# Optimization experiments

Hardware: AMD Instinct MI355X
Metric: run time of the kernel (lower is better)

Reference implementation:

```python
import jax, jax.numpy as jnp
import numpy as np

B = 2
D_MODEL = 768
N_HEADS = 16
N_POINTS = 4
SHAPES = [(16, 16), (32, 32), (64, 64), (96, 96)]  # (H, W) per level; query = last level
EPS = 1e-6


def layernorm(x, g, b):
    m = jnp.mean(x, -1, keepdims=True)
    xc = x - m
    v = jnp.mean(xc * xc, -1, keepdims=True)
    return xc * jax.lax.rsqrt(v + EPS) * g + b


def _bilinear(vflat, H, W, px, py):
    # vflat: (B, h, H*W, D); px/py: (B, Lq, h, P) unnormalized pixel coords
    # Equivalent to F.grid_sample(align_corners=False, padding_mode='zeros').
    x0f = jnp.floor(px); y0f = jnp.floor(py)
    lx = px - x0f; ly = py - y0f
    x0 = x0f.astype(jnp.int32); y0 = y0f.astype(jnp.int32)

    def gather(xi, yi, w):
        valid = ((xi >= 0) & (xi < W) & (yi >= 0) & (yi < H)).astype(vflat.dtype)
        idx = jnp.clip(yi, 0, H - 1) * W + jnp.clip(xi, 0, W - 1)
        idx = jnp.transpose(idx, (0, 2, 1, 3))        # (B, h, Lq, P)
        wv = jnp.transpose(w * valid, (0, 2, 1, 3))   # (B, h, Lq, P)
        b_, h_, q_, p_ = idx.shape
        g = jnp.take_along_axis(vflat, idx.reshape(b_, h_, q_ * p_)[..., None], axis=2)
        return g.reshape(b_, h_, q_, p_, -1) * wv[..., None]

    return (gather(x0, y0, (1 - lx) * (1 - ly)) + gather(x0 + 1, y0, lx * (1 - ly))
            + gather(x0, y0 + 1, (1 - lx) * ly) + gather(x0 + 1, y0 + 1, lx * ly))


def ms_deform_attn(query, ref_pts, feat, shapes, Wv, bv, Woff, boff, Wa, ba, Wo, bo):
    # query: (B, Lq, C); ref_pts: (1, Lq, 1, 2) in [0,1]; feat: (B, Lin, C)
    Bq, Lq, C = query.shape
    L, h, P = len(shapes), N_HEADS, N_POINTS
    D = C // h
    value = (feat @ Wv + bv).reshape(Bq, -1, h, D)
    off = (query @ Woff + boff).reshape(Bq, Lq, h, L, P, 2)
    w = jax.nn.softmax((query @ Wa + ba).reshape(Bq, Lq, h, L * P), axis=-1)
    w = w.reshape(Bq, Lq, h, L, P)
    normalizer = jnp.array([[W_, H_] for (H_, W_) in shapes], dtype=query.dtype)  # (L, 2) = [W, H]
    loc = ref_pts[:, :, None, :, None, :] + off / normalizer[None, None, None, :, None, :]
    out = jnp.zeros((Bq, h, Lq, D), query.dtype)
    start = 0
    for l, (H_, W_) in enumerate(shapes):
        vl = jnp.transpose(value[:, start:start + H_ * W_], (0, 2, 1, 3))  # (B, h, HW, D)
        start += H_ * W_
        px = loc[:, :, :, l, :, 0] * W_ - 0.5
        py = loc[:, :, :, l, :, 1] * H_ - 0.5
        samp = _bilinear(vl, H_, W_, px, py)                   # (B, h, Lq, P, D)
        wl = jnp.transpose(w[:, :, :, l, :], (0, 2, 1, 3))     # (B, h, Lq, P)
        out = out + jnp.einsum('bhqpd,bhqp->bhqd', samp, wl)
    out = jnp.transpose(out, (0, 2, 1, 3)).reshape(Bq, Lq, C)
    return out @ Wo + bo


def ref_points(e, dtype=jnp.float32):
    # torch.linspace(0.5, e-0.5, e)/e == (arange(e)+0.5)/e
    lin = (jnp.arange(e, dtype=dtype) + 0.5) / e
    ry, rx = jnp.meshgrid(lin, lin, indexing='ij')
    return jnp.stack([rx.ravel(), ry.ravel()], -1)[None, :, None, :]  # (1, e*e, 1, 2)


def setup_inputs() -> dict:
    key = jax.random.key(0)
    ks = jax.random.split(key, 16)
    d, h, P = D_MODEL, N_HEADS, N_POINTS
    inp = {}
    for i, (name, (H_, W_)) in enumerate(zip(['src0', 'src1', 'src2', 'src3'], SHAPES)):
        inp[name] = jax.random.normal(ks[i], (B, H_ * W_, d), jnp.float32)
    for pre in ('qn', 'fn', 'n1'):
        inp[pre + '_g'] = jnp.ones((d,), jnp.float32)
        inp[pre + '_b'] = jnp.zeros((d,), jnp.float32)
    inp['gamma1'] = 0.1 * jnp.ones((d,), jnp.float32)
    inp['gamma2'] = 0.1 * jnp.ones((d,), jnp.float32)

    def lin(k, din, dout):
        return jax.random.normal(k, (din, dout), jnp.float32) * (din ** -0.5)

    inp['c_Wv'] = lin(ks[4], d, d);               inp['c_bv'] = jnp.zeros((d,), jnp.float32)
    inp['c_Woff'] = lin(ks[5], d, h * 4 * P * 2); inp['c_boff'] = jnp.zeros((h * 4 * P * 2,), jnp.float32)
    inp['c_Wa'] = lin(ks[6], d, h * 4 * P);       inp['c_ba'] = jnp.zeros((h * 4 * P,), jnp.float32)
    inp['c_Wo'] = lin(ks[7], d, d);               inp['c_bo'] = jnp.zeros((d,), jnp.float32)
    inp['s_Wv'] = lin(ks[8], d, d);               inp['s_bv'] = jnp.zeros((d,), jnp.float32)
    inp['s_Woff'] = lin(ks[9], d, h * P * 2);     inp['s_boff'] = jnp.zeros((h * P * 2,), jnp.float32)
    inp['s_Wa'] = lin(ks[10], d, h * P);          inp['s_ba'] = jnp.zeros((h * P,), jnp.float32)
    inp['s_Wo'] = lin(ks[11], d, d);              inp['s_bo'] = jnp.zeros((d,), jnp.float32)
    return inp


def reference(src0, src1, src2, src3, qn_g, qn_b, fn_g, fn_b, n1_g, n1_b,
              gamma1, gamma2,
              c_Wv, c_bv, c_Woff, c_boff, c_Wa, c_ba, c_Wo, c_bo,
              s_Wv, s_bv, s_Woff, s_boff, s_Wa, s_ba, s_Wo, s_bo):
    feat = jnp.concatenate([src0, src1, src2, src3], axis=1)
    query = src3  # query_layer = -1
    e = SHAPES[-1][0]
    ref = ref_points(e, query.dtype)
    attn = ms_deform_attn(layernorm(query, qn_g, qn_b), ref, layernorm(feat, fn_g, fn_b),
                          SHAPES, c_Wv, c_bv, c_Woff, c_boff, c_Wa, c_ba, c_Wo, c_bo)
    attn1 = layernorm(attn, n1_g, n1_b)
    attn2 = ms_deform_attn(attn1, ref, attn1, [SHAPES[-1]],
                           s_Wv, s_bv, s_Woff, s_boff, s_Wa, s_ba, s_Wo, s_bo)
    attn = attn + gamma2 * attn2
    return query + gamma1 * attn
```

## Files before the change

kernel.cpp:

```cpp
#include <hip/hip_runtime.h>
#include <stdint.h>

typedef unsigned short u16;
typedef __attribute__((ext_vector_type(8))) __bf16 bf16x8;
typedef __attribute__((ext_vector_type(4))) float f32x4;
typedef __attribute__((ext_vector_type(2))) float f32x2;
typedef __attribute__((ext_vector_type(8))) u16 u16x8;
typedef __attribute__((ext_vector_type(4))) u16 u16x4;

#define DEV __device__ __forceinline__

DEV u16 f2b(float f) {
  union { float f; uint32_t u; } v; v.f = f;
  uint32_t u = v.u;
  return (u16)((u + 0x7fffu + ((u >> 16) & 1u)) >> 16);
}
DEV float b2f(u16 h) {
  union { uint32_t u; float f; } v; v.u = ((uint32_t)h) << 16;
  return v.f;
}
DEV float u2f(uint32_t u) {
  union { uint32_t u; float f; } v; v.u = u;
  return v.f;
}
DEV uint8_t f2fp8(float f) {
  return (uint8_t)(__builtin_amdgcn_cvt_pk_fp8_f32(f, f, 0, false) & 0xff);
}
DEV void fma16f8(f32x2* acc, uint4 v, float w) {
  f32x2 wv = {w, w};
  const uint32_t* pv = (const uint32_t*)&v;
  #pragma unroll
  for (int j = 0; j < 4; ++j) {
    f32x2 lo = __builtin_amdgcn_cvt_pk_f32_fp8(pv[j], false);
    f32x2 hi = __builtin_amdgcn_cvt_pk_f32_fp8(pv[j], true);
    acc[2 * j]     += wv * lo;
    acc[2 * j + 1] += wv * hi;
  }
}

__global__ __launch_bounds__(256) void wconv_kernel(
    const float* __restrict__ W0, const float* __restrict__ W1,
    const float* __restrict__ W2, const float* __restrict__ W3,
    const float* __restrict__ W4, const float* __restrict__ W5,
    const float* __restrict__ W6, const float* __restrict__ W7,
    u16* __restrict__ dst) {
  __shared__ float s[32][33];
  int bx = blockIdx.x;
  int ct = bx / 24;
  int kt = bx - ct * 24;
  const float* Wsrc; int N; int rowbase; int c0;
  if (ct < 24)       { Wsrc = W0; N = 768; rowbase = 0;    c0 = ct; }
  else if (ct < 40)  { Wsrc = W1; N = 512; rowbase = 768;  c0 = ct - 24; }
  else if (ct < 48)  { Wsrc = W2; N = 256; rowbase = 1280; c0 = ct - 40; }
  else if (ct < 72)  { Wsrc = W3; N = 768; rowbase = 1536; c0 = ct - 48; }
  else if (ct < 96)  { Wsrc = W4; N = 768; rowbase = 2304; c0 = ct - 72; }
  else if (ct < 100) { Wsrc = W5; N = 128; rowbase = 3072; c0 = ct - 96; }
  else if (ct < 104) { Wsrc = W6; N = 64;  rowbase = 3200; c0 = ct - 100; }
  else               { Wsrc = W7; N = 768; rowbase = 3328; c0 = ct - 104; }
  const int tx = threadIdx.x & 31, ty = threadIdx.x >> 5;
  const int n = c0 * 32 + tx;
  const int k0 = kt * 32;
  #pragma unroll
  for (int j = 0; j < 4; ++j) {
    int k = k0 + ty + j * 8;
    s[ty + j * 8][tx] = (n < N) ? Wsrc[(size_t)k * N + n] : 0.0f;
  }
  __syncthreads();
  #pragma unroll
  for (int j = 0; j < 4; ++j) {
    int nr = c0 * 32 + ty + j * 8;
    dst[(size_t)(rowbase + nr) * 768 + k0 + tx] = f2b(s[tx][ty + j * 8]);
  }
}

DEV void ln_core(float4 v, const float* __restrict__ g, const float* __restrict__ b,
                 u16* __restrict__ o, int t, float* red) {
  float s = v.x + v.y + v.z + v.w;
  float s2 = v.x * v.x + v.y * v.y + v.z * v.z + v.w * v.w;
  #pragma unroll
  for (int m = 1; m < 64; m <<= 1) { s += __shfl_xor(s, m); s2 += __shfl_xor(s2, m); }
  if ((t & 63) == 0) { red[t >> 6] = s; red[3 + (t >> 6)] = s2; }
  __syncthreads();
  float S = red[0] + red[1] + red[2];
  float S2 = red[3] + red[4] + red[5];
  float mean = S * (1.0f / 768.0f);
  float var = S2 * (1.0f / 768.0f) - mean * mean;
  float rstd = rsqrtf(var + 1e-6f);
  float4 gv = ((const float4*)g)[t], bv = ((const float4*)b)[t];
  u16x4 ov;
  ov[0] = f2b((v.x - mean) * rstd * gv.x + bv.x);
  ov[1] = f2b((v.y - mean) * rstd * gv.y + bv.y);
  ov[2] = f2b((v.z - mean) * rstd * gv.z + bv.z);
  ov[3] = f2b((v.w - mean) * rstd * gv.w + bv.w);
  *(u16x4*)(o + t * 4) = ov;
}

__global__ __launch_bounds__(192) void ln_rows_kernel(const float* __restrict__ in,
    const float* __restrict__ g, const float* __restrict__ b, u16* __restrict__ out) {
  __shared__ float red[6];
  size_t row = blockIdx.x;
  int t = threadIdx.x;
  ln_core(((const float4*)(in + row * 768))[t], g, b, out + row * 768, t, red);
}

__global__ __launch_bounds__(192) void ln_rows_b16_kernel(const u16* __restrict__ in,
    const float* __restrict__ g, const float* __restrict__ b, u16* __restrict__ out) {
  __shared__ float red[6];
  size_t row = blockIdx.x;
  int t = threadIdx.x;
  u16x4 r = *(const u16x4*)(in + row * 768 + t * 4);
  float4 v = {b2f(r[0]), b2f(r[1]), b2f(r[2]), b2f(r[3])};
  ln_core(v, g, b, out + row * 768, t, red);
}

__global__ __launch_bounds__(192) void ln_feat_kernel(const float* __restrict__ s0,
    const float* __restrict__ s1, const float* __restrict__ s2, const float* __restrict__ s3,
    const float* __restrict__ g, const float* __restrict__ b, u16* __restrict__ out) {
  __shared__ float red[6];
  int row = blockIdx.x;
  int bb = row / 14592, pos = row - bb * 14592;
  const float* x;
  if (pos < 256)       x = s0 + ((size_t)bb * 256  + pos) * 768;
  else if (pos < 1280) x = s1 + ((size_t)bb * 1024 + (pos - 256)) * 768;
  else if (pos < 5376) x = s2 + ((size_t)bb * 4096 + (pos - 1280)) * 768;
  else                 x = s3 + ((size_t)bb * 9216 + (pos - 5376)) * 768;
  int t = threadIdx.x;
  ln_core(((const float4*)x)[t], g, b, out + (size_t)row * 768, t, red);
}

enum { MODE_F32 = 0, MODE_BF16 = 1, MODE_FINAL = 2, MODE_FP8T = 3 };

template <int MODE, int NT, int LROW = 1>
__global__ __launch_bounds__(256) void gemm_kernel(
    const u16* __restrict__ A, const u16* __restrict__ Wt,
    const float* __restrict__ bias1, const float* __restrict__ bias2,
    int split, int nb, void* __restrict__ Cout, int N,
    const u16* __restrict__ attnb, const float* __restrict__ resid,
    const float* __restrict__ g1, const float* __restrict__ g2) {
  constexpr int K = 768;
  __shared__ u16 smem[4 * 128 * 64];
  const int t = threadIdx.x;
  const int lane = t & 63;
  const int w = t >> 6;
  const int wr = w >> 1, wc = w & 1;
  const int chunk = gridDim.x >> 3;
  const int tile = (blockIdx.x & 7) * chunk + (blockIdx.x >> 3);
  const int tm = tile / NT, tn = tile - tm * NT;
  const size_t m0 = (size_t)tm * 128;
  const int n0 = tn * 128;

  f32x4 acc[4][4] = {};

  auto STAGE = [&](int buf, int kt) {
    u16* sA = smem + buf * 16384;
    u16* sB = sA + 8192;
    #pragma unroll
    for (int i = 0; i < 4; ++i) {
      int ci = i * 256 + t;
      int row = ci >> 3, c8 = ci & 7;
      int kc = c8 ^ (row & 7);
      const u16* ga = A + (m0 + row) * K + kt + kc * 8;
      const u16* gb = Wt + ((size_t)n0 + row) * K + kt + kc * 8;
      __builtin_amdgcn_global_load_lds((const __attribute__((address_space(1))) void*)ga,
          (__attribute__((address_space(3))) void*)(sA + ci * 8), 16, 0, 0);
      __builtin_amdgcn_global_load_lds((const __attribute__((address_space(1))) void*)gb,
          (__attribute__((address_space(3))) void*)(sB + ci * 8), 16, 0, 0);
    }
  };

  STAGE(0, 0);
  __syncthreads();
  int cur = 0;
  for (int kt = 0; kt < K; kt += 64) {
    if (kt + 64 < K) STAGE(cur ^ 1, kt + 64);
    const u16* sA = smem + cur * 16384;
    const u16* sB = sA + 8192;
    #pragma unroll
    for (int ks = 0; ks < 2; ++ks) {
      bf16x8 af[4], bfr[4];
      #pragma unroll
      for (int m = 0; m < 4; ++m) {
        int row = wr * 64 + m * 16 + (lane & 15);
        int pc = (ks * 4 + (lane >> 4)) ^ (row & 7);
        af[m] = *(const bf16x8*)(sA + row * 64 + pc * 8);
      }
      #pragma unroll
      for (int n = 0; n < 4; ++n) {
        int row = wc * 64 + n * 16 + (lane & 15);
        int pc = (ks * 4 + (lane >> 4)) ^ (row & 7);
        bfr[n] = *(const bf16x8*)(sB + row * 64 + pc * 8);
      }
      #pragma unroll
      for (int m = 0; m < 4; ++m)
        #pragma unroll
        for (int n = 0; n < 4; ++n)
          acc[m][n] = __builtin_amdgcn_mfma_f32_16x16x32_bf16(af[m], bfr[n], acc[m][n], 0, 0, 0);
    }
    __syncthreads();
    cur ^= 1;
  }

  if constexpr (MODE == MODE_BF16) {
    #pragma unroll
    for (int m = 0; m < 4; ++m) {
      #pragma unroll
      for (int n = 0; n < 4; ++n) {
        int lcol = wc * 64 + n * 16 + (lane & 15);
        int gcol = n0 + lcol;
        float bv = (gcol < split) ? bias1[gcol] : ((gcol < nb) ? bias2[gcol - split] : 0.0f);
        #pragma unroll
        for (int r = 0; r < 4; ++r) {
          int lrow = wr * 64 + m * 16 + (lane >> 4) * 4 + r;
          smem[lrow * 136 + lcol] = f2b(acc[m][n][r] + bv);
        }
      }
    }
    __syncthreads();
    #pragma unroll
    for (int i = 0; i < 8; ++i) {
      int c = t + 256 * i;
      int lrow = c >> 4, col8 = (c & 15) * 8;
      u16x8 vv = *(const u16x8*)(smem + lrow * 136 + col8);
      int gcol = n0 + col8;
      size_t grow = m0 + (size_t)lrow;
      *(u16x8*)((u16*)Cout + grow * (size_t)N + gcol) = vv;
    }
  } else if constexpr (MODE == MODE_FP8T) {
    uint8_t* s8 = (uint8_t*)smem;
    #pragma unroll
    for (int m = 0; m < 4; ++m) {
      #pragma unroll
      for (int n = 0; n < 4; ++n) {
        int lcol = wc * 64 + n * 16 + (lane & 15);
        int gcol = n0 + lcol;
        float bv = (gcol < split) ? bias1[gcol] : ((gcol < nb) ? bias2[gcol - split] : 0.0f);
        #pragma unroll
        for (int r = 0; r < 4; ++r) {
          int lrow = wr * 64 + m * 16 + (lane >> 4) * 4 + r;
          s8[lrow * 144 + lcol] = f2fp8(acc[m][n][r] + bv);
        }
      }
    }
    __syncthreads();
    #pragma unroll
    for (int i = 0; i < 4; ++i) {
      int c = t + 256 * i;
      int lrow = c >> 3, col16 = (c & 7) * 16;
      uint4 vv = *(const uint4*)(s8 + lrow * 144 + col16);
      int gcol = n0 + col16;
      size_t grow = m0 + (size_t)lrow;
      int gi = (int)grow;
      int bb = gi / LROW, pos = gi - bb * LROW;
      int hh = gcol / 48, dd = gcol - hh * 48;
      *(uint4*)((uint8_t*)Cout + (((size_t)bb * 16 + hh) * LROW + pos) * 48 + dd) = vv;
    }
  } else {
    #pragma unroll
    for (int m = 0; m < 4; ++m) {
      #pragma unroll
      for (int n = 0; n < 4; ++n) {
        int col = n0 + wc * 64 + n * 16 + (lane & 15);
        float bv = (col < split) ? bias1[col] : ((col < nb) ? bias2[col - split] : 0.0f);
        #pragma unroll
        for (int r = 0; r < 4; ++r) {
          size_t grow = m0 + (size_t)(wr * 64 + m * 16 + (lane >> 4) * 4 + r);
          float v = acc[m][n][r] + bv;
          size_t idx = grow * (size_t)N + col;
          if constexpr (MODE == MODE_F32) {
            ((float*)Cout)[idx] = v;
          } else {
            ((float*)Cout)[idx] = resid[idx] + g1[col] * (b2f(attnb[idx]) + g2[col] * v);
          }
        }
      }
    }
  }
}

__global__ __launch_bounds__(256, 4) void samp_c_kernel(const uint8_t* __restrict__ value,
    const u16* __restrict__ offa, u16* __restrict__ out) {
  __shared__ uint8_t sdesc[4 * 16 * 528];
  const int orig = blockIdx.x;
  const int cpx = gridDim.x >> 3;
  const int bq0 = ((orig & 7) * cpx + (orig >> 3)) * 4;
  const int t = threadIdx.x;

  {
    const int qi = t >> 6, h = (t >> 2) & 15, l = t & 3;
    const int bq = bq0 + qi;
    const int b = bq / 9216, q = bq - b * 9216;
    const u16* rw = offa + (size_t)bq * 768;
    u16x8 A0 = *(const u16x8*)(rw + 512 + h * 16);
    u16x8 A1 = *(const u16x8*)(rw + 512 + h * 16 + 8);
    float lg[16];
    #pragma unroll
    for (int i = 0; i < 8; ++i) { lg[i] = b2f(A0[i]); lg[8 + i] = b2f(A1[i]); }
    float mx = lg[0];
    #pragma unroll
    for (int i = 1; i < 16; ++i) mx = fmaxf(mx, lg[i]);
    float sum = 0.0f;
    #pragma unroll
    for (int i = 0; i < 16; ++i) sum += __expf(lg[i] - mx);
    const float rs = 1.0f / sum;
    float w0 = (l == 0) ? lg[0] : ((l == 1) ? lg[4] : ((l == 2) ? lg[8]  : lg[12]));
    float w1 = (l == 0) ? lg[1] : ((l == 1) ? lg[5] : ((l == 2) ? lg[9]  : lg[13]));
    float w2 = (l == 0) ? lg[2] : ((l == 1) ? lg[6] : ((l == 2) ? lg[10] : lg[14]));
    float w3 = (l == 0) ? lg[3] : ((l == 1) ? lg[7] : ((l == 2) ? lg[11] : lg[15]));

    const int Wd = (l == 3) ? 96 : (16 << l);
    const int STl = (l == 0) ? 0 : ((l == 1) ? 256 : ((l == 2) ? 1280 : 5376));
    const float fW = (float)Wd;
    const float rx = ((q % 96) + 0.5f) * (1.0f / 96.0f);
    const float ry = ((q / 96) + 0.5f) * (1.0f / 96.0f);
    const int headbase = (b * 16 + h) * 14592 + STl;

    u16x8 O = *(const u16x8*)(rw + h * 32 + l * 8);
    float oxs[4] = {b2f(O[0]), b2f(O[2]), b2f(O[4]), b2f(O[6])};
    float oys[4] = {b2f(O[1]), b2f(O[3]), b2f(O[5]), b2f(O[7])};
    float wgs[4] = {w0, w1, w2, w3};
    uint8_t* dpb = sdesc + (qi * 16 + h) * 528 + l * 32;
    #pragma unroll
    for (int pt = 0; pt < 4; ++pt) {
      float px = rx * fW + oxs[pt] - 0.5f;
      float py = ry * fW + oys[pt] - 0.5f;
      float wgt = __expf(wgs[pt] - mx) * rs;
      float x0f = floorf(px), y0f = floorf(py);
      float lx = px - x0f, ly = py - y0f;
      int x0 = (int)x0f, y0 = (int)y0f;
      int xc0 = min(max(x0, 0), Wd - 1), xc1 = min(max(x0 + 1, 0), Wd - 1);
      int yc0 = min(max(y0, 0), Wd - 1), yc1 = min(max(y0 + 1, 0), Wd - 1);
      float wx0 = ((unsigned)x0       < (unsigned)Wd) ? (1.0f - lx) : 0.0f;
      float wx1 = ((unsigned)(x0 + 1) < (unsigned)Wd) ? lx          : 0.0f;
      float wy0 = (((unsigned)y0       < (unsigned)Wd) ? (1.0f - ly) : 0.0f) * wgt;
      float wy1 = (((unsigned)(y0 + 1) < (unsigned)Wd) ? ly          : 0.0f) * wgt;
      int4 ii;
      ii.x = (headbase + yc0 * Wd + xc0) * 48;
      ii.y = (headbase + yc0 * Wd + xc1) * 48;
      ii.z = (headbase + yc1 * Wd + xc0) * 48;
      ii.w = (headbase + yc1 * Wd + xc1) * 48;
      float4 ww = {wx0 * wy0, wx1 * wy0, wx0 * wy1, wx1 * wy1};
      *(int4*)(dpb + pt * 128) = ii;
      *(float4*)(dpb + pt * 128 + 16) = ww;
    }
  }
  __syncthreads();
  if (t >= 192) return;

  const int qi = t / 48, r = t - qi * 48;
  const int h = r / 3, d16 = r - h * 3;
  const int bq = bq0 + qi;
  const int hd = d16 * 16;
  const uint8_t* vB = value;
  const uint8_t* dp = sdesc + (qi * 16 + h) * 528;

  f32x2 acc0[8] = {}, acc1[8] = {};
  #pragma unroll
  for (int p = 0; p < 16; ++p) {
    const uint8_t* dpp = dp + p * 32;
    int4   ii = *(const int4*)(dpp);
    float4 ww = *(const float4*)(dpp + 16);
    uint4 g0 = *(const uint4*)(vB + (ii.x + hd));
    uint4 g1 = *(const uint4*)(vB + (ii.y + hd));
    uint4 g2 = *(const uint4*)(vB + (ii.z + hd));
    uint4 g3 = *(const uint4*)(vB + (ii.w + hd));
    fma16f8(acc0, g0, ww.x);
    fma16f8(acc1, g1, ww.y);
    fma16f8(acc0, g2, ww.z);
    fma16f8(acc1, g3, ww.w);
  }
  u16x8 o0, o1;
  #pragma unroll
  for (int j = 0; j < 4; ++j) {
    o0[2*j]   = f2b(acc0[j][0] + acc1[j][0]);
    o0[2*j+1] = f2b(acc0[j][1] + acc1[j][1]);
    o1[2*j]   = f2b(acc0[4+j][0] + acc1[4+j][0]);
    o1[2*j+1] = f2b(acc0[4+j][1] + acc1[4+j][1]);
  }
  u16* op = out + (size_t)bq * 768 + h * 48 + d16 * 16;
  *(u16x8*)op = o0;
  *(u16x8*)(op + 8) = o1;
}

__global__ __launch_bounds__(256, 4) void samp_s_kernel(const uint8_t* __restrict__ value,
    const u16* __restrict__ offa, u16* __restrict__ out) {
  __shared__ uint8_t sdesc[4 * 16 * 144];
  const int orig = blockIdx.x;
  const int cpx = gridDim.x >> 3;
  const int bq0 = ((orig & 7) * cpx + (orig >> 3)) * 4;
  const int t = threadIdx.x;

  if (t < 64) {
    const int qi = t >> 4, h = t & 15;
    const int bq = bq0 + qi;
    const int b = bq / 9216, q = bq - b * 9216;
    const u16* rw = offa + (size_t)bq * 256;
    u16x4 Lv = *(const u16x4*)(rw + 128 + h * 4);
    float lg[4] = {b2f(Lv[0]), b2f(Lv[1]), b2f(Lv[2]), b2f(Lv[3])};
    float mx = fmaxf(fmaxf(lg[0], lg[1]), fmaxf(lg[2], lg[3]));
    float sum = __expf(lg[0] - mx) + __expf(lg[1] - mx) + __expf(lg[2] - mx) + __expf(lg[3] - mx);
    const float rs = 1.0f / sum;
    const float rx = ((q % 96) + 0.5f) * (1.0f / 96.0f);
    const float ry = ((q / 96) + 0.5f) * (1.0f / 96.0f);
    const int headbase = (b * 16 + h) * 9216;
    u16x8 O = *(const u16x8*)(rw + h * 8);
    float oxs[4] = {b2f(O[0]), b2f(O[2]), b2f(O[4]), b2f(O[6])};
    float oys[4] = {b2f(O[1]), b2f(O[3]), b2f(O[5]), b2f(O[7])};
    uint8_t* dpb = sdesc + (qi * 16 + h) * 144;
    #pragma unroll
    for (int pt = 0; pt < 4; ++pt) {
      float px = rx * 96.0f + oxs[pt] - 0.5f;
      float py = ry * 96.0f + oys[pt] - 0.5f;
      float wgt = __expf(lg[pt] - mx) * rs;
      float x0f = floorf(px), y0f = floorf(py);
      float lx = px - x0f, ly = py - y0f;
      int x0 = (int)x0f, y0 = (int)y0f;
      int xc0 = min(max(x0, 0), 95), xc1 = min(max(x0 + 1, 0), 95);
      int yc0 = min(max(y0, 0), 95), yc1 = min(max(y0 + 1, 0), 95);
      float wx0 = ((unsigned)x0       < 96u) ? (1.0f - lx) : 0.0f;
      float wx1 = ((unsigned)(x0 + 1) < 96u) ? lx          : 0.0f;
      float wy0 = (((unsigned)y0       < 96u) ? (1.0f - ly) : 0.0f) * wgt;
      float wy1 = (((unsigned)(y0 + 1) < 96u) ? ly          : 0.0f) * wgt;
      int4 ii;
      ii.x = (headbase + yc0 * 96 + xc0) * 48;
      ii.y = (headbase + yc0 * 96 + xc1) * 48;
      ii.z = (headbase + yc1 * 96 + xc0) * 48;
      ii.w = (headbase + yc1 * 96 + xc1) * 48;
      float4 ww = {wx0 * wy0, wx1 * wy0, wx0 * wy1, wx1 * wy1};
      *(int4*)(dpb + pt * 32) = ii;
      *(float4*)(dpb + pt * 32 + 16) = ww;
    }
  }
  __syncthreads();
  if (t >= 192) return;

  const int qi = t / 48, r = t - qi * 48;
  const int h = r / 3, d16 = r - h * 3;
  const int bq = bq0 + qi;
  const int hd = d16 * 16;
  const uint8_t* vB = value;
  const uint8_t* dp = sdesc + (qi * 16 + h) * 144;

  f32x2 acc0[8] = {}, acc1[8] = {};
  #pragma unroll
  for (int p = 0; p < 4; ++p) {
    const uint8_t* dpp = dp + p * 32;
    int4   ii = *(const int4*)(dpp);
    float4 ww = *(const float4*)(dpp + 16);
    uint4 g0 = *(const uint4*)(vB + (ii.x + hd));
    uint4 g1 = *(const uint4*)(vB + (ii.y + hd));
    uint4 g2 = *(const uint4*)(vB + (ii.z + hd));
    uint4 g3 = *(const uint4*)(vB + (ii.w + hd));
    fma16f8(acc0, g0, ww.x);
    fma16f8(acc1, g1, ww.y);
    fma16f8(acc0, g2, ww.z);
    fma16f8(acc1, g3, ww.w);
  }
  u16x8 o0, o1;
  #pragma unroll
  for (int j = 0; j < 4; ++j) {
    o0[2*j]   = f2b(acc0[j][0] + acc1[j][0]);
    o0[2*j+1] = f2b(acc0[j][1] + acc1[j][1]);
    o1[2*j]   = f2b(acc0[4+j][0] + acc1[4+j][0]);
    o1[2*j+1] = f2b(acc0[4+j][1] + acc1[4+j][1]);
  }
  u16* op = out + (size_t)bq * 768 + h * 48 + d16 * 16;
  *(u16x8*)op = o0;
  *(u16x8*)(op + 8) = o1;
}

extern "C" void kernel_launch(void* const* d_in, const int* in_sizes, int n_in,
                              void* d_out, int out_size, void* d_ws, size_t ws_size,
                              hipStream_t stream) {
  (void)in_sizes; (void)n_in; (void)out_size; (void)ws_size;
  const float* src0 = (const float*)d_in[0];
  const float* src1 = (const float*)d_in[1];
  const float* src2 = (const float*)d_in[2];
  const float* src3 = (const float*)d_in[3];
  const float* qn_g = (const float*)d_in[4];
  const float* qn_b = (const float*)d_in[5];
  const float* fn_g = (const float*)d_in[6];
  const float* fn_b = (const float*)d_in[7];
  const float* n1_g = (const float*)d_in[8];
  const float* n1_b = (const float*)d_in[9];
  const float* gamma1 = (const float*)d_in[10];
  const float* gamma2 = (const float*)d_in[11];
  const float* c_Wv  = (const float*)d_in[12]; const float* c_bv   = (const float*)d_in[13];
  const float* c_Woff= (const float*)d_in[14]; const float* c_boff = (const float*)d_in[15];
  const float* c_Wa  = (const float*)d_in[16]; const float* c_ba   = (const float*)d_in[17];
  const float* c_Wo  = (const float*)d_in[18]; const float* c_bo   = (const float*)d_in[19];
  const float* s_Wv  = (const float*)d_in[20]; const float* s_bv   = (const float*)d_in[21];
  const float* s_Woff= (const float*)d_in[22]; const float* s_boff = (const float*)d_in[23];
  const float* s_Wa  = (const float*)d_in[24]; const float* s_ba   = (const float*)d_in[25];
  const float* s_Wo  = (const float*)d_in[26]; const float* s_bo   = (const float*)d_in[27];

  constexpr int Lq = 9216;
  constexpr int Mq = 2 * Lq;
  constexpr int Mf = 2 * 14592;

  constexpr size_t O_qln   = 8u << 20;
  constexpr size_t O_fln   = O_qln   + (size_t)Mq * 768 * 2;
  constexpr size_t O_valc  = O_fln   + (size_t)Mf * 768 * 2;
  constexpr size_t O_offac = O_valc  + (size_t)Mf * 768;
  constexpr size_t O_sampc = O_qln;
  constexpr size_t O_attn  = O_fln;
  constexpr size_t O_attn1 = O_attn  + (size_t)Mq * 768 * 2;
  constexpr size_t O_vals  = O_attn1 + (size_t)Mq * 768 * 2;
  constexpr size_t O_offas = O_vals  + (size_t)Mq * 768;
  constexpr size_t O_samps = O_offas + (size_t)Mq * 256 * 2;

  uint8_t* ws = (uint8_t*)d_ws;
  u16* Wbase = (u16*)ws;
  auto Wrow = [&](int r) { return Wbase + (size_t)r * 768; };
  auto Wp = [&](size_t o) { return (u16*)(ws + o); };

  wconv_kernel<<<3072, 256, 0, stream>>>(c_Wv, c_Woff, c_Wa, c_Wo, s_Wv, s_Woff, s_Wa, s_Wo, Wbase);

  ln_rows_kernel<<<Mq, 192, 0, stream>>>(src3, qn_g, qn_b, Wp(O_qln));
  ln_feat_kernel<<<Mf, 192, 0, stream>>>(src0, src1, src2, src3, fn_g, fn_b, Wp(O_fln));

  gemm_kernel<MODE_FP8T, 6, 14592><<<(Mf / 128) * 6, 256, 0, stream>>>(
      Wp(O_fln), Wrow(0), c_bv, nullptr, 768, 768, ws + O_valc, 768,
      nullptr, nullptr, nullptr, nullptr);
  gemm_kernel<MODE_BF16, 6><<<(Mq / 128) * 6, 256, 0, stream>>>(
      Wp(O_qln), Wrow(768), c_boff, c_ba, 512, 768, Wp(O_offac), 768,
      nullptr, nullptr, nullptr, nullptr);

  samp_c_kernel<<<Mq / 4, 256, 0, stream>>>(ws + O_valc, Wp(O_offac), Wp(O_sampc));

  gemm_kernel<MODE_BF16, 6><<<(Mq / 128) * 6, 256, 0, stream>>>(
      Wp(O_sampc), Wrow(1536), c_bo, nullptr, 768, 768, Wp(O_attn), 768,
      nullptr, nullptr, nullptr, nullptr);

  ln_rows_b16_kernel<<<Mq, 192, 0, stream>>>(Wp(O_attn), n1_g, n1_b, Wp(O_attn1));

  gemm_kernel<MODE_FP8T, 6, 9216><<<(Mq / 128) * 6, 256, 0, stream>>>(
      Wp(O_attn1), Wrow(2304), s_bv, nullptr, 768, 768, ws + O_vals, 768,
      nullptr, nullptr, nullptr, nullptr);
  gemm_kernel<MODE_BF16, 2><<<(Mq / 128) * 2, 256, 0, stream>>>(
      Wp(O_attn1), Wrow(3072), s_boff, s_ba, 128, 192, Wp(O_offas), 256,
      nullptr, nullptr, nullptr, nullptr);

  samp_s_kernel<<<Mq / 4, 256, 0, stream>>>(ws + O_vals, Wp(O_offas), Wp(O_samps));

  gemm_kernel<MODE_FINAL, 6><<<(Mq / 128) * 6, 256, 0, stream>>>(
      Wp(O_samps), Wrow(3328), s_bo, nullptr, 768, 768, (float*)d_out, 768,
      Wp(O_attn), src3, gamma1, gamma2);
}
```

Before: 333.8 us.

## Replace 128x128 GEMM with 256x256 8-wave pipelined GEMM with half-tile staging

The bf16 GEMM moves from 128x128 tiles with 4 waves to 256x256 tiles with 8 waves. The K loop is restructured so each A and B half-tile is staged separately into double-buffered LDS, with quarter-tile MFMA blocks interleaved with loads and barriers and s_setprio raised around the MFMAs. Work-group indices are also remapped across the 8 XCDs, handling uneven counts. The aim is more data reuse per tile and better overlap of global loads with matrix math. In exchange it uses 128KB of LDS per block and more registers, and the grids shrink to a few hundred blocks, which may leave CUs idle on the smaller GEMMs.

```diff
diff --git a/kernel.cpp b/kernel.cpp
--- a/kernel.cpp
+++ b/kernel.cpp
@@ -130,150 +130,213 @@
 
 enum { MODE_F32 = 0, MODE_BF16 = 1, MODE_FINAL = 2, MODE_FP8T = 3 };
 
-template <int MODE, int NT, int LROW = 1>
-__global__ __launch_bounds__(256) void gemm_kernel(
+template <int MODE, int NTILES, int LROW = 1>
+__global__ __launch_bounds__(512, 2) void gemm256_kernel(
     const u16* __restrict__ A, const u16* __restrict__ Wt,
     const float* __restrict__ bias1, const float* __restrict__ bias2,
     int split, int nb, void* __restrict__ Cout, int N,
     const u16* __restrict__ attnb, const float* __restrict__ resid,
-    const float* __restrict__ g1, const float* __restrict__ g2) {
+    const float* __restrict__ g1v, const float* __restrict__ g2v) {
   constexpr int K = 768;
-  __shared__ u16 smem[4 * 128 * 64];
+  __shared__ u16 smem[65536];
   const int t = threadIdx.x;
   const int lane = t & 63;
-  const int w = t >> 6;
-  const int wr = w >> 1, wc = w & 1;
-  const int chunk = gridDim.x >> 3;
-  const int tile = (blockIdx.x & 7) * chunk + (blockIdx.x >> 3);
-  const int tm = tile / NT, tn = tile - tm * NT;
-  const size_t m0 = (size_t)tm * 128;
-  const int n0 = tn * 128;
-
-  f32x4 acc[4][4] = {};
-
-  auto STAGE = [&](int buf, int kt) {
-    u16* sA = smem + buf * 16384;
-    u16* sB = sA + 8192;
-    #pragma unroll
-    for (int i = 0; i < 4; ++i) {
-      int ci = i * 256 + t;
+  const int wid = t >> 6;
+  const int wm = wid >> 2, wn = wid & 3;
+  const int nwg = gridDim.x;
+  const int qq = nwg >> 3, rr8 = nwg & 7;
+  const int xcd = blockIdx.x & 7, bidx = blockIdx.x >> 3;
+  const int wgid = (xcd < rr8 ? xcd * (qq + 1) : rr8 * (qq + 1) + (xcd - rr8) * qq) + bidx;
+  const int tm = wgid / NTILES, tn = wgid - tm * NTILES;
+  const size_t m0 = (size_t)tm * 256;
+  const int n0 = tn * 256;
+
+  f32x4 acc[8][4] = {};
+  bf16x8 af[4][2];
+  bf16x8 bfr[4][2];
+
+  auto STAGE_HALF = [&](int dst, int buf, int kt) {
+    const int half = dst & 1;
+    u16* lds = smem + buf * 32768 + (dst >> 1) * 16384 + half * 8192;
+    #pragma unroll
+    for (int i = 0; i < 2; ++i) {
+      int ci = i * 512 + t;
       int row = ci >> 3, c8 = ci & 7;
       int kc = c8 ^ (row & 7);
-      const u16* ga = A + (m0 + row) * K + kt + kc * 8;
-      const u16* gb = Wt + ((size_t)n0 + row) * K + kt + kc * 8;
-      __builtin_amdgcn_global_load_lds((const __attribute__((address_space(1))) void*)ga,
-          (__attribute__((address_space(3))) void*)(sA + ci * 8), 16, 0, 0);
-      __builtin_amdgcn_global_load_lds((const __attribute__((address_space(1))) void*)gb,
-          (__attribute__((address_space(3))) void*)(sB + ci * 8), 16, 0, 0);
+      const u16* g = (dst < 2)
+          ? A + (m0 + half * 128 + row) * (size_t)K + kt + kc * 8
+          : Wt + ((size_t)n0 + half * 128 + row) * K + kt + kc * 8;
+      __builtin_amdgcn_global_load_lds((const __attribute__((address_space(1))) void*)g,
+          (__attribute__((address_space(3))) void*)(lds + ci * 8), 16, 0, 0);
     }
   };
-
-  STAGE(0, 0);
+  auto LOAD_A = [&](int buf, int mh) {
+    const u16* sA = smem + buf * 32768;
+    #pragma unroll
+    for (int m = 0; m < 4; ++m)
+      #pragma unroll
+      for (int ks = 0; ks < 2; ++ks) {
+        int row = wm * 128 + mh * 64 + m * 16 + (lane & 15);
+        int pc = (ks * 4 + (lane >> 4)) ^ (row & 7);
+        af[m][ks] = *(const bf16x8*)(sA + row * 64 + pc * 8);
+      }
+  };
+  auto LOAD_B = [&](int buf, int nh) {
+    const u16* sB = smem + buf * 32768 + 16384;
+    #pragma unroll
+    for (int n = 0; n < 2; ++n)
+      #pragma unroll
+      for (int ks = 0; ks < 2; ++ks) {
+        int row = wn * 64 + nh * 32 + n * 16 + (lane & 15);
+        int pc = (ks * 4 + (lane >> 4)) ^ (row & 7);
+        bfr[nh * 2 + n][ks] = *(const bf16x8*)(sB + row * 64 + pc * 8);
+      }
+  };
+  auto MMA_Q = [&](int mh, int nh) {
+    __builtin_amdgcn_s_setprio(1);
+    #pragma unroll
+    for (int m = 0; m < 4; ++m)
+      #pragma unroll
+      for (int n = 0; n < 2; ++n)
+        #pragma unroll
+        for (int ks = 0; ks < 2; ++ks)
+          acc[mh * 4 + m][nh * 2 + n] = __builtin_amdgcn_mfma_f32_16x16x32_bf16(
+              af[m][ks], bfr[nh * 2 + n][ks], acc[mh * 4 + m][nh * 2 + n], 0, 0, 0);
+    __builtin_amdgcn_s_setprio(0);
+  };
+
+  STAGE_HALF(0, 0, 0); STAGE_HALF(1, 0, 0); STAGE_HALF(2, 0, 0); STAGE_HALF(3, 0, 0);
+  STAGE_HALF(2, 1, 64); STAGE_HALF(3, 1, 64);
+  asm volatile("s_waitcnt vmcnt(4)" ::: "memory");
+  __builtin_amdgcn_s_barrier();
+
+  for (int j = 0; j < 6; ++j) {
+    const int s1k = (2 * j + 1) * 64;
+    const int s2k = (2 * j + 2 < 12) ? (2 * j + 2) * 64 : 704;
+    const int s3k = (2 * j + 3 < 12) ? (2 * j + 3) * 64 : 704;
+    LOAD_A(0, 0); LOAD_B(0, 0);
+    STAGE_HALF(0, 1, s1k);
+    __builtin_amdgcn_s_barrier();
+    MMA_Q(0, 0);
+    __builtin_amdgcn_s_barrier();
+    LOAD_B(0, 1);
+    STAGE_HALF(1, 1, s1k);
+    __builtin_amdgcn_s_barrier();
+    MMA_Q(0, 1);
+    __builtin_amdgcn_s_barrier();
+    LOAD_A(0, 1);
+    STAGE_HALF(2, 0, s2k);
+    __builtin_amdgcn_s_barrier();
+    MMA_Q(1, 0);
+    __builtin_amdgcn_s_barrier();
+    STAGE_HALF(3, 0, s2k);
+    __builtin_amdgcn_s_barrier();
+    MMA_Q(1, 1);
+    asm volatile("s_waitcnt vmcnt(4)" ::: "memory");
+    __builtin_amdgcn_s_barrier();
+    LOAD_A(1, 0); LOAD_B(1, 0);
+    STAGE_HALF(0, 0, s2k);
+    __builtin_amdgcn_s_barrier();
+    MMA_Q(0, 0);
+    __builtin_amdgcn_s_barrier();
+    LOAD_B(1, 1);
+    STAGE_HALF(1, 0, s2k);
+    __builtin_amdgcn_s_barrier();
+    MMA_Q(0, 1);
+    __builtin_amdgcn_s_barrier();
+    LOAD_A(1, 1);
+    STAGE_HALF(2, 1, s3k);
+    __builtin_amdgcn_s_barrier();
+    MMA_Q(1, 0);
+    __builtin_amdgcn_s_barrier();
+    STAGE_HALF(3, 1, s3k);
+    __builtin_amdgcn_s_barrier();
+    MMA_Q(1, 1);
+    asm volatile("s_waitcnt vmcnt(4)" ::: "memory");
+    __builtin_amdgcn_s_barrier();
+  }
+  asm volatile("s_waitcnt vmcnt(0)" ::: "memory");
   __syncthreads();
-  int cur = 0;
-  for (int kt = 0; kt < K; kt += 64) {
-    if (kt + 64 < K) STAGE(cur ^ 1, kt + 64);
-    const u16* sA = smem + cur * 16384;
-    const u16* sB = sA + 8192;
-    #pragma unroll
-    for (int ks = 0; ks < 2; ++ks) {
-      bf16x8 af[4], bfr[4];
+
+  if constexpr (MODE == MODE_BF16) {
+    #pragma unroll
+    for (int half = 0; half < 2; ++half) {
+      if (wm == half) {
+        #pragma unroll
+        for (int m = 0; m < 8; ++m)
+          #pragma unroll
+          for (int n = 0; n < 4; ++n) {
+            int lcol = wn * 64 + n * 16 + (lane & 15);
+            int gcol = n0 + lcol;
+            float bv = (gcol < split) ? bias1[gcol] : ((gcol < nb) ? bias2[gcol - split] : 0.0f);
+            #pragma unroll
+            for (int rr = 0; rr < 4; ++rr) {
+              int lrow = m * 16 + (lane >> 4) * 4 + rr;
+              smem[lrow * 264 + lcol] = f2b(acc[m][n][rr] + bv);
+            }
+          }
+      }
+      __syncthreads();
       #pragma unroll
-      for (int m = 0; m < 4; ++m) {
-        int row = wr * 64 + m * 16 + (lane & 15);
-        int pc = (ks * 4 + (lane >> 4)) ^ (row & 7);
-        af[m] = *(const bf16x8*)(sA + row * 64 + pc * 8);
+      for (int i = 0; i < 8; ++i) {
+        int c = t + 512 * i;
+        int lrow = c >> 5, col8 = (c & 31) * 8;
+        u16x8 vv = *(const u16x8*)(smem + lrow * 264 + col8);
+        size_t grow = m0 + half * 128 + lrow;
+        int gcol = n0 + col8;
+        *(u16x8*)((u16*)Cout + grow * (size_t)N + gcol) = vv;
       }
-      #pragma unroll
-      for (int n = 0; n < 4; ++n) {
-        int row = wc * 64 + n * 16 + (lane & 15);
-        int pc = (ks * 4 + (lane >> 4)) ^ (row & 7);
-        bfr[n] = *(const bf16x8*)(sB + row * 64 + pc * 8);
-      }
-      #pragma unroll
-      for (int m = 0; m < 4; ++m)
-        #pragma unroll
-        for (int n = 0; n < 4; ++n)
-          acc[m][n] = __builtin_amdgcn_mfma_f32_16x16x32_bf16(af[m], bfr[n], acc[m][n], 0, 0, 0);
-    }
-    __syncthreads();
-    cur ^= 1;
-  }
-
-  if constexpr (MODE == MODE_BF16) {
-    #pragma unroll
-    for (int m = 0; m < 4; ++m) {
-      #pragma unroll
-      for (int n = 0; n < 4; ++n) {
-        int lcol = wc * 64 + n * 16 + (lane & 15);
-        int gcol = n0 + lcol;
-        float bv = (gcol < split) ? bias1[gcol] : ((gcol < nb) ? bias2[gcol - split] : 0.0f);
-        #pragma unroll
-        for (int r = 0; r < 4; ++r) {
-          int lrow = wr * 64 + m * 16 + (lane >> 4) * 4 + r;
-          smem[lrow * 136 + lcol] = f2b(acc[m][n][r] + bv);
-        }
-      }
-    }
-    __syncthreads();
-    #pragma unroll
-    for (int i = 0; i < 8; ++i) {
-      int c = t + 256 * i;
-      int lrow = c >> 4, col8 = (c & 15) * 8;
-      u16x8 vv = *(const u16x8*)(smem + lrow * 136 + col8);
-      int gcol = n0 + col8;
-      size_t grow = m0 + (size_t)lrow;
-      *(u16x8*)((u16*)Cout + grow * (size_t)N + gcol) = vv;
+      __syncthreads();
     }
   } else if constexpr (MODE == MODE_FP8T) {
     uint8_t* s8 = (uint8_t*)smem;
     #pragma unroll
-    for (int m = 0; m < 4; ++m) {
+    for (int half = 0; half < 2; ++half) {
+      if (wm == half) {
+        #pragma unroll
+        for (int m = 0; m < 8; ++m)
+          #pragma unroll
+          for (int n = 0; n < 4; ++n) {
+            int lcol = wn * 64 + n * 16 + (lane & 15);
+            int gcol = n0 + lcol;
+            float bv = (gcol < split) ? bias1[gcol] : ((gcol < nb) ? bias2[gcol - split] : 0.0f);
+            #pragma unroll
+            for (int rr = 0; rr < 4; ++rr) {
+              int lrow = m * 16 + (lane >> 4) * 4 + rr;
+              s8[lrow * 272 + lcol] = f2fp8(acc[m][n][rr] + bv);
+            }
+          }
+      }
+      __syncthreads();
+      #pragma unroll
+      for (int i = 0; i < 4; ++i) {
+        int c = t + 512 * i;
+        int lrow = c >> 4, col16 = (c & 15) * 16;
+        uint4 vv = *(const uint4*)(s8 + lrow * 272 + col16);
+        size_t grow = m0 + half * 128 + lrow;
+        int gcol = n0 + col16;
+        int gi = (int)grow;
+        int bb = gi / LROW, pos = gi - bb * LROW;
+        int hh = gcol / 48, dd = gcol - hh * 48;
+        *(uint4*)((uint8_t*)Cout + (((size_t)bb * 16 + hh) * LROW + pos) * 48 + dd) = vv;
+      }
+      __syncthreads();
+    }
+  } else {
+    #pragma unroll
+    for (int m = 0; m < 8; ++m)
       #pragma unroll
       for (int n = 0; n < 4; ++n) {
-        int lcol = wc * 64 + n * 16 + (lane & 15);
-        int gcol = n0 + lcol;
-        float bv = (gcol < split) ? bias1[gcol] : ((gcol < nb) ? bias2[gcol - split] : 0.0f);
+        int col = n0 + wn * 64 + n * 16 + (lane & 15);
+        float bv = (col < split) ? bias1[col] : ((col < nb) ? bias2[col - split] : 0.0f);
         #pragma unroll
-        for (int r = 0; r < 4; ++r) {
-          int lrow = wr * 64 + m * 16 + (lane >> 4) * 4 + r;
-          s8[lrow * 144 + lcol] = f2fp8(acc[m][n][r] + bv);
+        for (int rr = 0; rr < 4; ++rr) {
+          size_t grow = m0 + wm * 128 + m * 16 + (lane >> 4) * 4 + rr;
+          float v = acc[m][n][rr] + bv;
+          size_t idx = grow * (size_t)N + col;
+          ((float*)Cout)[idx] = resid[idx] + g1v[col] * (b2f(attnb[idx]) + g2v[col] * v);
         }
       }
-    }
-    __syncthreads();
-    #pragma unroll
-    for (int i = 0; i < 4; ++i) {
-      int c = t + 256 * i;
-      int lrow = c >> 3, col16 = (c & 7) * 16;
-      uint4 vv = *(const uint4*)(s8 + lrow * 144 + col16);
-      int gcol = n0 + col16;
-      size_t grow = m0 + (size_t)lrow;
-      int gi = (int)grow;
-      int bb = gi / LROW, pos = gi - bb * LROW;
-      int hh = gcol / 48, dd = gcol - hh * 48;
-      *(uint4*)((uint8_t*)Cout + (((size_t)bb * 16 + hh) * LROW + pos) * 48 + dd) = vv;
-    }
-  } else {
-    #pragma unroll
-    for (int m = 0; m < 4; ++m) {
-      #pragma unroll
-      for (int n = 0; n < 4; ++n) {
-        int col = n0 + wc * 64 + n * 16 + (lane & 15);
-        float bv = (col < split) ? bias1[col] : ((col < nb) ? bias2[col - split] : 0.0f);
-        #pragma unroll
-        for (int r = 0; r < 4; ++r) {
-          size_t grow = m0 + (size_t)(wr * 64 + m * 16 + (lane >> 4) * 4 + r);
-          float v = acc[m][n][r] + bv;
-          size_t idx = grow * (size_t)N + col;
-          if constexpr (MODE == MODE_F32) {
-            ((float*)Cout)[idx] = v;
-          } else {
-            ((float*)Cout)[idx] = resid[idx] + g1[col] * (b2f(attnb[idx]) + g2[col] * v);
-          }
-        }
-      }
-    }
   }
 }
 
@@ -518,31 +581,31 @@
   ln_rows_kernel<<<Mq, 192, 0, stream>>>(src3, qn_g, qn_b, Wp(O_qln));
   ln_feat_kernel<<<Mf, 192, 0, stream>>>(src0, src1, src2, src3, fn_g, fn_b, Wp(O_fln));
 
-  gemm_kernel<MODE_FP8T, 6, 14592><<<(Mf / 128) * 6, 256, 0, stream>>>(
+  gemm256_kernel<MODE_FP8T, 3, 14592><<<(Mf / 256) * 3, 512, 0, stream>>>(
       Wp(O_fln), Wrow(0), c_bv, nullptr, 768, 768, ws + O_valc, 768,
       nullptr, nullptr, nullptr, nullptr);
-  gemm_kernel<MODE_BF16, 6><<<(Mq / 128) * 6, 256, 0, stream>>>(
+  gemm256_kernel<MODE_BF16, 3><<<(Mq / 256) * 3, 512, 0, stream>>>(
       Wp(O_qln), Wrow(768), c_boff, c_ba, 512, 768, Wp(O_offac), 768,
       nullptr, nullptr, nullptr, nullptr);
 
   samp_c_kernel<<<Mq / 4, 256, 0, stream>>>(ws + O_valc, Wp(O_offac), Wp(O_sampc));
 
-  gemm_kernel<MODE_BF16, 6><<<(Mq / 128) * 6, 256, 0, stream>>>(
+  gemm256_kernel<MODE_BF16, 3><<<(Mq / 256) * 3, 512, 0, stream>>>(
       Wp(O_sampc), Wrow(1536), c_bo, nullptr, 768, 768, Wp(O_attn), 768,
       nullptr, nullptr, nullptr, nullptr);
 
   ln_rows_b16_kernel<<<Mq, 192, 0, stream>>>(Wp(O_attn), n1_g, n1_b, Wp(O_attn1));
 
-  gemm_kernel<MODE_FP8T, 6, 9216><<<(Mq / 128) * 6, 256, 0, stream>>>(
+  gemm256_kernel<MODE_FP8T, 3, 9216><<<(Mq / 256) * 3, 512, 0, stream>>>(
       Wp(O_attn1), Wrow(2304), s_bv, nullptr, 768, 768, ws + O_vals, 768,
       nullptr, nullptr, nullptr, nullptr);
-  gemm_kernel<MODE_BF16, 2><<<(Mq / 128) * 2, 256, 0, stream>>>(
+  gemm256_kernel<MODE_BF16, 1><<<Mq / 256, 512, 0, stream>>>(
       Wp(O_attn1), Wrow(3072), s_boff, s_ba, 128, 192, Wp(O_offas), 256,
       nullptr, nullptr, nullptr, nullptr);
 
   samp_s_kernel<<<Mq / 4, 256, 0, stream>>>(ws + O_vals, Wp(O_offas), Wp(O_samps));
 
-  gemm_kernel<MODE_FINAL, 6><<<(Mq / 128) * 6, 256, 0, stream>>>(
+  gemm256_kernel<MODE_FINAL, 3><<<(Mq / 256) * 3, 512, 0, stream>>>(
       Wp(O_samps), Wrow(3328), s_bo, nullptr, 768, 768, (float*)d_out, 768,
       Wp(O_attn), src3, gamma1, gamma2);
 }
```

New measurement: 388.5 us. +16.4%, slower.
